# Kernel optimization log

Hardware: AMD Instinct MI355X
Metric: run time of the kernel (lower is better)

Reference implementation:

```python
import jax, jax.numpy as jnp
import numpy as np

N0, N1, N2 = 200000, 50000, 12500
E0, E1, E2 = 3200000, 800000, 200000
CIN, C, COUT = 4, 128, 1


def gcn(x, W, b, src, dst, n):
    # GCN conv with added self-loops and symmetric degree normalization
    h = x @ W
    loops = jnp.arange(n)
    s = jnp.concatenate([src, loops])
    d = jnp.concatenate([dst, loops])
    deg = jax.ops.segment_sum(jnp.ones(s.shape[0], h.dtype), d, num_segments=n)
    inv = jax.lax.rsqrt(jnp.maximum(deg, 1.0))
    msg = h[s] * (inv[s] * inv[d])[:, None]
    return jax.ops.segment_sum(msg, d, num_segments=n) + b


def pool_max(x, clusters, n_clusters):
    # cluster-based max pooling; empty clusters -> 0
    p = jax.ops.segment_max(x, clusters, num_segments=n_clusters)
    return jnp.where(jnp.isneginf(p), jnp.zeros_like(p), p)


def setup_inputs() -> dict:
    ks = jax.random.split(jax.random.key(0), 40)

    def w(k, i, o):
        return jax.random.normal(k, (i, o), jnp.float32) / np.float32(np.sqrt(i))

    inp = {
        'x': jax.random.normal(ks[0], (N0, CIN), jnp.float32),
        'edge_index0': jax.random.randint(ks[1], (2, E0), 0, N0),
        'edge_index1': jax.random.randint(ks[2], (2, E1), 0, N1),
        'edge_index2': jax.random.randint(ks[3], (2, E2), 0, N2),
        'clusters0': jax.random.randint(ks[4], (N0,), 0, N1),
        'clusters1': jax.random.randint(ks[5], (N1,), 0, N2),
        # encoder level 0
        'w_e0a': w(ks[6], CIN, C), 'b_e0a': jnp.zeros((C,), jnp.float32),
        'w_e0b': w(ks[7], C, C),   'b_e0b': jnp.zeros((C,), jnp.float32),
        # encoder level 1
        'w_e1a': w(ks[8], C, C),   'b_e1a': jnp.zeros((C,), jnp.float32),
        'w_e1b': w(ks[9], C, C),   'b_e1b': jnp.zeros((C,), jnp.float32),
        # bottom level 2
        'w_ba': w(ks[10], C, C),   'b_ba': jnp.zeros((C,), jnp.float32),
        'w_bb': w(ks[11], C, C),   'b_bb': jnp.zeros((C,), jnp.float32),
        # decoder level 1 (concat skip -> 2C in)
        'w_d1a': w(ks[12], 2 * C, C), 'b_d1a': jnp.zeros((C,), jnp.float32),
        'w_d1b': w(ks[13], C, C),     'b_d1b': jnp.zeros((C,), jnp.float32),
        # decoder level 0
        'w_d0a': w(ks[14], 2 * C, C), 'b_d0a': jnp.zeros((C,), jnp.float32),
        'w_d0b': w(ks[15], C, C),     'b_d0b': jnp.zeros((C,), jnp.float32),
        # output projection
        'w_out': w(ks[16], C, COUT), 'b_out': jnp.zeros((COUT,), jnp.float32),
    }
    return inp


def reference(x, edge_index0, edge_index1, edge_index2, clusters0, clusters1,
              w_e0a, b_e0a, w_e0b, b_e0b, w_e1a, b_e1a, w_e1b, b_e1b,
              w_ba, b_ba, w_bb, b_bb, w_d1a, b_d1a, w_d1b, b_d1b,
              w_d0a, b_d0a, w_d0b, b_d0b, w_out, b_out):
    n0 = x.shape[0]
    n1 = clusters1.shape[0]
    n2 = N2
    relu = jax.nn.relu
    s0, d0 = edge_index0[0], edge_index0[1]
    s1, d1 = edge_index1[0], edge_index1[1]
    s2, d2 = edge_index2[0], edge_index2[1]

    # encoder level 0
    e0 = relu(gcn(x, w_e0a, b_e0a, s0, d0, n0))
    e0 = relu(gcn(e0, w_e0b, b_e0b, s0, d0, n0))
    # pool -> level 1
    x1 = pool_max(e0, clusters0, n1)
    e1 = relu(gcn(x1, w_e1a, b_e1a, s1, d1, n1))
    e1 = relu(gcn(e1, w_e1b, b_e1b, s1, d1, n1))
    # pool -> level 2 (bottom)
    x2 = pool_max(e1, clusters1, n2)
    bt = relu(gcn(x2, w_ba, b_ba, s2, d2, n2))
    bt = relu(gcn(bt, w_bb, b_bb, s2, d2, n2))
    # unpool -> level 1, concat skip
    u1 = jnp.concatenate([bt[clusters1], e1], axis=1)
    dl1 = relu(gcn(u1, w_d1a, b_d1a, s1, d1, n1))
    dl1 = relu(gcn(dl1, w_d1b, b_d1b, s1, d1, n1))
    # unpool -> level 0, concat skip
    u0 = jnp.concatenate([dl1[clusters0], e0], axis=1)
    dl0 = relu(gcn(u0, w_d0a, b_d0a, s0, d0, n0))
    dl0 = relu(gcn(dl0, w_d0b, b_d0b, s0, d0, n0))
    # per-node output head
    return dl0 @ w_out + b_out
```

## Files before the change

### kernel.cpp

```cpp
#include <hip/hip_runtime.h>
#include <hip/hip_fp16.h>
#include <cstdint>
#include <cstddef>

#define PN0 200000
#define PN1 50000
#define PN2 12500
#define PE0 3200000
#define PE1 800000
#define PE2 200000

#define GCAP 64
#define CCAP 32

static inline int cdiv_i(int a, int b) { return (a + b - 1) / b; }

union H4 { uint4 q; uint2 u; __half2 h[2]; };

typedef _Float16 f16x8 __attribute__((ext_vector_type(8)));
typedef float f32x4 __attribute__((ext_vector_type(4)));
union F8 { uint4 q; f16x8 f; };

__device__ inline float2 load2f(const float* p) { return *(const float2*)p; }
__device__ inline float2 load2f(const __half* p) { return __half22float2(*(const __half2*)p); }


struct SegInfo {
    const int* idx[5];
    const int* src[3];
    int item_off[5];
    int cnt_off[5];
    int col_base[5];
    int cap[5];
    int total;
};

__global__ __launch_bounds__(256) void build_all_k(SegInfo s, int* __restrict__ cnt,
                                                   int* __restrict__ col) {
    int i = blockIdx.x * 256 + threadIdx.x;
    if (i >= s.total) return;
    int seg = 0;
#pragma unroll
    for (int t = 1; t < 5; ++t) if (i >= s.item_off[t]) seg = t;
    int il = i - s.item_off[seg];
    int d = s.idx[seg][il];
    int slot = atomicAdd(&cnt[s.cnt_off[seg] + d], 1);
    int cap = s.cap[seg];
    if (slot < cap) {
        int val = (seg < 3) ? s.src[seg][il] : il;
        col[s.col_base[seg] + d * cap + slot] = val;
    }
}

__global__ __launch_bounds__(256) void inv_all_k(const int* __restrict__ cnt, float* __restrict__ inv,
                                                 int c0, int c1, int c2) {
    int i = blockIdx.x * 256 + threadIdx.x;
    int total = PN0 + PN1 + PN2;
    if (i >= total) return;
    int coff, il;
    if (i < PN0) { coff = c0; il = i; }
    else if (i < PN0 + PN1) { coff = c1; il = i - PN0; }
    else { coff = c2; il = i - PN0 - PN1; }
    inv[i] = rsqrtf((float)(cnt[coff + il] + 1));
}

struct PrepW { const float* src[11]; __half* dst[11]; };
__global__ __launch_bounds__(256) void prep_w_k(PrepW p) {
    const float* w = p.src[blockIdx.x];
    __half* o = p.dst[blockIdx.x];
    for (int i = threadIdx.x; i < 16384; i += 256) {
        int k = i >> 7, n = i & 127;
        o[n * 128 + k] = __float2half(w[i]);
    }
}


__global__ __launch_bounds__(256) void agg4_k(const float* __restrict__ X, float* __restrict__ O,
                                              const int* __restrict__ deg, const int* __restrict__ col,
                                              const float* __restrict__ inv, int N) {
    int v = blockIdx.x * 256 + threadIdx.x;
    if (v >= N) return;
    float iv = inv[v];
    float4 xv = *(const float4*)(X + (size_t)v * 4);
    float ax = xv.x * iv, ay = xv.y * iv, az = xv.z * iv, aw = xv.w * iv;
    int b0 = v * GCAP, b1 = b0 + deg[v];
    for (int j = b0; j < b1; ++j) {
        int u = col[j];
        float iu = inv[u];
        float4 xu = *(const float4*)(X + (size_t)u * 4);
        ax += xu.x * iu; ay += xu.y * iu; az += xu.z * iu; aw += xu.w * iu;
    }
    float4 o; o.x = ax * iv; o.y = ay * iv; o.z = az * iv; o.w = aw * iv;
    *(float4*)(O + (size_t)v * 4) = o;
}

__global__ __launch_bounds__(256) void gemm4_k(const float* __restrict__ XA, const float* __restrict__ W,
                                               const float* __restrict__ bias, __half* __restrict__ O, int N) {
    int wid = (blockIdx.x * 256 + threadIdx.x) >> 6;
    int lane = threadIdx.x & 63;
    if (wid >= N) return;
    float4 x = *(const float4*)(XA + (size_t)wid * 4);
    int c = lane * 2;
    float2 w0 = *(const float2*)(W + c);
    float2 w1 = *(const float2*)(W + 128 + c);
    float2 w2 = *(const float2*)(W + 256 + c);
    float2 w3 = *(const float2*)(W + 384 + c);
    float2 b = *(const float2*)(bias + c);
    float ox = b.x + x.x * w0.x + x.y * w1.x + x.z * w2.x + x.w * w3.x;
    float oy = b.y + x.x * w0.y + x.y * w1.y + x.z * w2.y + x.w * w3.y;
    ox = fmaxf(ox, 0.f); oy = fmaxf(oy, 0.f);
    *(__half2*)(O + (size_t)wid * 128 + c) = __floats2half2_rn(ox, oy);
}

__global__ __launch_bounds__(256) void agg_k(const __half* __restrict__ H, __half* __restrict__ O,
                                             const int* __restrict__ deg, const int* __restrict__ col,
                                             const float* __restrict__ inv, const float* __restrict__ bias,
                                             int N) {
    int wpair = (blockIdx.x * 256 + threadIdx.x) >> 6;
    int lane = threadIdx.x & 63;
    int v = wpair * 2 + (lane >> 5);
    int l32 = lane & 31;
    if (v >= N) return;
    float iv = inv[v];
    int c4 = l32 * 4;
    float4 a0 = {0,0,0,0}, a1 = {0,0,0,0}, a2 = {0,0,0,0}, a3 = {0,0,0,0};
    int b0 = v * GCAP, b1 = b0 + deg[v];
    int j = b0;
    for (; j + 8 <= b1; j += 8) {
        int u0 = col[j],     u1 = col[j + 1], u2 = col[j + 2], u3 = col[j + 3];
        int u4 = col[j + 4], u5 = col[j + 5], u6 = col[j + 6], u7 = col[j + 7];
        H4 t0, t1, t2, t3, t4, t5, t6, t7;
        t0.u = *(const uint2*)(H + (size_t)u0 * 128 + c4);
        t1.u = *(const uint2*)(H + (size_t)u1 * 128 + c4);
        t2.u = *(const uint2*)(H + (size_t)u2 * 128 + c4);
        t3.u = *(const uint2*)(H + (size_t)u3 * 128 + c4);
        t4.u = *(const uint2*)(H + (size_t)u4 * 128 + c4);
        t5.u = *(const uint2*)(H + (size_t)u5 * 128 + c4);
        t6.u = *(const uint2*)(H + (size_t)u6 * 128 + c4);
        t7.u = *(const uint2*)(H + (size_t)u7 * 128 + c4);
        float2 p, q;
        p = __half22float2(t0.h[0]); q = __half22float2(t0.h[1]);
        a0.x += p.x; a0.y += p.y; a0.z += q.x; a0.w += q.y;
        p = __half22float2(t1.h[0]); q = __half22float2(t1.h[1]);
        a1.x += p.x; a1.y += p.y; a1.z += q.x; a1.w += q.y;
        p = __half22float2(t2.h[0]); q = __half22float2(t2.h[1]);
        a2.x += p.x; a2.y += p.y; a2.z += q.x; a2.w += q.y;
        p = __half22float2(t3.h[0]); q = __half22float2(t3.h[1]);
        a3.x += p.x; a3.y += p.y; a3.z += q.x; a3.w += q.y;
        p = __half22float2(t4.h[0]); q = __half22float2(t4.h[1]);
        a0.x += p.x; a0.y += p.y; a0.z += q.x; a0.w += q.y;
        p = __half22float2(t5.h[0]); q = __half22float2(t5.h[1]);
        a1.x += p.x; a1.y += p.y; a1.z += q.x; a1.w += q.y;
        p = __half22float2(t6.h[0]); q = __half22float2(t6.h[1]);
        a2.x += p.x; a2.y += p.y; a2.z += q.x; a2.w += q.y;
        p = __half22float2(t7.h[0]); q = __half22float2(t7.h[1]);
        a3.x += p.x; a3.y += p.y; a3.z += q.x; a3.w += q.y;
    }
    for (; j + 4 <= b1; j += 4) {
        int u0 = col[j], u1 = col[j + 1], u2 = col[j + 2], u3 = col[j + 3];
        H4 t0, t1, t2, t3;
        t0.u = *(const uint2*)(H + (size_t)u0 * 128 + c4);
        t1.u = *(const uint2*)(H + (size_t)u1 * 128 + c4);
        t2.u = *(const uint2*)(H + (size_t)u2 * 128 + c4);
        t3.u = *(const uint2*)(H + (size_t)u3 * 128 + c4);
        float2 p, q;
        p = __half22float2(t0.h[0]); q = __half22float2(t0.h[1]);
        a0.x += p.x; a0.y += p.y; a0.z += q.x; a0.w += q.y;
        p = __half22float2(t1.h[0]); q = __half22float2(t1.h[1]);
        a1.x += p.x; a1.y += p.y; a1.z += q.x; a1.w += q.y;
        p = __half22float2(t2.h[0]); q = __half22float2(t2.h[1]);
        a2.x += p.x; a2.y += p.y; a2.z += q.x; a2.w += q.y;
        p = __half22float2(t3.h[0]); q = __half22float2(t3.h[1]);
        a3.x += p.x; a3.y += p.y; a3.z += q.x; a3.w += q.y;
    }
    for (; j < b1; ++j) {
        H4 t; t.u = *(const uint2*)(H + (size_t)col[j] * 128 + c4);
        float2 p = __half22float2(t.h[0]), q = __half22float2(t.h[1]);
        a0.x += p.x; a0.y += p.y; a0.z += q.x; a0.w += q.y;
    }
    {
        H4 t; t.u = *(const uint2*)(H + (size_t)v * 128 + c4);
        float2 p = __half22float2(t.h[0]), q = __half22float2(t.h[1]);
        a1.x += p.x; a1.y += p.y; a1.z += q.x; a1.w += q.y;
    }
    float4 s;
    s.x = (a0.x + a1.x) + (a2.x + a3.x);
    s.y = (a0.y + a1.y) + (a2.y + a3.y);
    s.z = (a0.z + a1.z) + (a2.z + a3.z);
    s.w = (a0.w + a1.w) + (a2.w + a3.w);
    float4 b = *(const float4*)(bias + c4);
    H4 t;
    t.h[0] = __floats2half2_rn(fmaxf(s.x * iv + b.x, 0.f), fmaxf(s.y * iv + b.y, 0.f));
    t.h[1] = __floats2half2_rn(fmaxf(s.z * iv + b.z, 0.f), fmaxf(s.w * iv + b.w, 0.f));
    *(uint2*)(O + (size_t)v * 128 + c4) = t.u;
}

__global__ __launch_bounds__(256) void agg_head_k(const __half* __restrict__ H,
                                                  const int* __restrict__ deg, const int* __restrict__ col,
                                                  const float* __restrict__ inv, const float* __restrict__ bias,
                                                  const float* __restrict__ wout, const float* __restrict__ bout,
                                                  float* __restrict__ out, int N) {
    int wpair = (blockIdx.x * 256 + threadIdx.x) >> 6;
    int lane = threadIdx.x & 63;
    int v = wpair * 2 + (lane >> 5);
    int l32 = lane & 31;
    if (v >= N) return;
    float iv = inv[v];
    int c4 = l32 * 4;
    float4 a0 = {0,0,0,0}, a1 = {0,0,0,0}, a2 = {0,0,0,0}, a3 = {0,0,0,0};
    int b0 = v * GCAP, b1 = b0 + deg[v];
    int j = b0;
    for (; j + 8 <= b1; j += 8) {
        int u0 = col[j],     u1 = col[j + 1], u2 = col[j + 2], u3 = col[j + 3];
        int u4 = col[j + 4], u5 = col[j + 5], u6 = col[j + 6], u7 = col[j + 7];
        H4 t0, t1, t2, t3, t4, t5, t6, t7;
        t0.u = *(const uint2*)(H + (size_t)u0 * 128 + c4);
        t1.u = *(const uint2*)(H + (size_t)u1 * 128 + c4);
        t2.u = *(const uint2*)(H + (size_t)u2 * 128 + c4);
        t3.u = *(const uint2*)(H + (size_t)u3 * 128 + c4);
        t4.u = *(const uint2*)(H + (size_t)u4 * 128 + c4);
        t5.u = *(const uint2*)(H + (size_t)u5 * 128 + c4);
        t6.u = *(const uint2*)(H + (size_t)u6 * 128 + c4);
        t7.u = *(const uint2*)(H + (size_t)u7 * 128 + c4);
        float2 p, q;
        p = __half22float2(t0.h[0]); q = __half22float2(t0.h[1]);
        a0.x += p.x; a0.y += p.y; a0.z += q.x; a0.w += q.y;
        p = __half22float2(t1.h[0]); q = __half22float2(t1.h[1]);
        a1.x += p.x; a1.y += p.y; a1.z += q.x; a1.w += q.y;
        p = __half22float2(t2.h[0]); q = __half22float2(t2.h[1]);
        a2.x += p.x; a2.y += p.y; a2.z += q.x; a2.w += q.y;
        p = __half22float2(t3.h[0]); q = __half22float2(t3.h[1]);
        a3.x += p.x; a3.y += p.y; a3.z += q.x; a3.w += q.y;
        p = __half22float2(t4.h[0]); q = __half22float2(t4.h[1]);
        a0.x += p.x; a0.y += p.y; a0.z += q.x; a0.w += q.y;
        p = __half22float2(t5.h[0]); q = __half22float2(t5.h[1]);
        a1.x += p.x; a1.y += p.y; a1.z += q.x; a1.w += q.y;
        p = __half22float2(t6.h[0]); q = __half22float2(t6.h[1]);
        a2.x += p.x; a2.y += p.y; a2.z += q.x; a2.w += q.y;
        p = __half22float2(t7.h[0]); q = __half22float2(t7.h[1]);
        a3.x += p.x; a3.y += p.y; a3.z += q.x; a3.w += q.y;
    }
    for (; j + 4 <= b1; j += 4) {
        int u0 = col[j], u1 = col[j + 1], u2 = col[j + 2], u3 = col[j + 3];
        H4 t0, t1, t2, t3;
        t0.u = *(const uint2*)(H + (size_t)u0 * 128 + c4);
        t1.u = *(const uint2*)(H + (size_t)u1 * 128 + c4);
        t2.u = *(const uint2*)(H + (size_t)u2 * 128 + c4);
        t3.u = *(const uint2*)(H + (size_t)u3 * 128 + c4);
        float2 p, q;
        p = __half22float2(t0.h[0]); q = __half22float2(t0.h[1]);
        a0.x += p.x; a0.y += p.y; a0.z += q.x; a0.w += q.y;
        p = __half22float2(t1.h[0]); q = __half22float2(t1.h[1]);
        a1.x += p.x; a1.y += p.y; a1.z += q.x; a1.w += q.y;
        p = __half22float2(t2.h[0]); q = __half22float2(t2.h[1]);
        a2.x += p.x; a2.y += p.y; a2.z += q.x; a2.w += q.y;
        p = __half22float2(t3.h[0]); q = __half22float2(t3.h[1]);
        a3.x += p.x; a3.y += p.y; a3.z += q.x; a3.w += q.y;
    }
    for (; j < b1; ++j) {
        H4 t; t.u = *(const uint2*)(H + (size_t)col[j] * 128 + c4);
        float2 p = __half22float2(t.h[0]), q = __half22float2(t.h[1]);
        a0.x += p.x; a0.y += p.y; a0.z += q.x; a0.w += q.y;
    }
    {
        H4 t; t.u = *(const uint2*)(H + (size_t)v * 128 + c4);
        float2 p = __half22float2(t.h[0]), q = __half22float2(t.h[1]);
        a1.x += p.x; a1.y += p.y; a1.z += q.x; a1.w += q.y;
    }
    float4 sm;
    sm.x = (a0.x + a1.x) + (a2.x + a3.x);
    sm.y = (a0.y + a1.y) + (a2.y + a3.y);
    sm.z = (a0.z + a1.z) + (a2.z + a3.z);
    sm.w = (a0.w + a1.w) + (a2.w + a3.w);
    float4 b = *(const float4*)(bias + c4);
    float4 w = *(const float4*)(wout + c4);
    float s = fmaxf(sm.x * iv + b.x, 0.f) * w.x
            + fmaxf(sm.y * iv + b.y, 0.f) * w.y
            + fmaxf(sm.z * iv + b.z, 0.f) * w.z
            + fmaxf(sm.w * iv + b.w, 0.f) * w.w;
    for (int off = 16; off >= 1; off >>= 1) s += __shfl_down(s, off, 32);
    if (l32 == 0) out[v] = s + bout[0];
}

__global__ __launch_bounds__(256) void pool_k(const __half* __restrict__ X, __half* __restrict__ O,
                                              const int* __restrict__ cdeg, const int* __restrict__ col,
                                              int Nc) {
    int wid = (blockIdx.x * 256 + threadIdx.x) >> 6;
    int lane = threadIdx.x & 63;
    if (wid >= Nc) return;
    int c = lane * 2;
    float mx = 0.f, my = 0.f;
    int b0 = wid * CCAP, b1 = b0 + cdeg[wid];
    for (int j = b0; j < b1; ++j) {
        int u = col[j];
        float2 t = load2f(X + (size_t)u * 128 + c);
        mx = fmaxf(mx, t.x); my = fmaxf(my, t.y);
    }
    *(__half2*)(O + (size_t)wid * 128 + c) = __floats2half2_rn(mx, my);
}

__global__ __launch_bounds__(256) void gemm_mfma_k(const __half* __restrict__ X, const __half* __restrict__ Wt,
                                                   __half* __restrict__ O, int N,
                                                   const int* __restrict__ cl, const __half* __restrict__ T,
                                                   const float* __restrict__ rowscale) {
    __shared__ __half Ws[128 * 136];
    int tid = threadIdx.x;
    for (int i = tid; i < 2048; i += 256) {
        int n = i >> 4, k = (i & 15) * 8;
        *(uint4*)(&Ws[n * 136 + k]) = *(const uint4*)(Wt + n * 128 + k);
    }
    __syncthreads();

    int wave = tid >> 6, lane = tid & 63;
    int quad = lane >> 4, m = lane & 15;
    int rowBase = blockIdx.x * 64 + wave * 16;
    int arow = rowBase + m;
    bool aok = arow < N;

    f16x8 afr[4];
    const __half* xrow = X + (size_t)arow * 128;
#pragma unroll
    for (int kc = 0; kc < 4; ++kc) {
        F8 t;
        if (aok) t.q = *(const uint4*)(xrow + kc * 32 + quad * 8);
        else { t.q.x = 0; t.q.y = 0; t.q.z = 0; t.q.w = 0; }
        afr[kc] = t.f;
    }

    f32x4 acc[8];
#pragma unroll
    for (int t = 0; t < 8; ++t) acc[t] = (f32x4){0.f, 0.f, 0.f, 0.f};

#pragma unroll
    for (int kc = 0; kc < 4; ++kc) {
#pragma unroll
        for (int t = 0; t < 8; ++t) {
            F8 b;
            b.q = *(const uint4*)(&Ws[(t * 16 + m) * 136 + kc * 32 + quad * 8]);
            acc[t] = __builtin_amdgcn_mfma_f32_16x16x32_f16(afr[kc], b.f, acc[t], 0, 0, 0);
        }
    }

    int baseRow = rowBase + quad * 4;
#pragma unroll
    for (int r = 0; r < 4; ++r) {
        int orow = baseRow + r;
        if (orow >= N) continue;
        float rs = rowscale ? rowscale[orow] : 1.0f;
        const __half* Trow = cl ? (T + (size_t)cl[orow] * 128) : nullptr;
#pragma unroll
        for (int t = 0; t < 8; ++t) {
            float v = acc[t][r];
            if (Trow) v += __half2float(Trow[t * 16 + m]);
            O[(size_t)orow * 128 + t * 16 + m] = __float2half(v * rs);
        }
    }
}


extern "C" void kernel_launch(void* const* d_in, const int* in_sizes, int n_in,
                              void* d_out, int out_size, void* d_ws, size_t ws_size,
                              hipStream_t stream) {
    const float* x        = (const float*)d_in[0];
    const int*   ei0      = (const int*)d_in[1];
    const int*   ei1      = (const int*)d_in[2];
    const int*   ei2      = (const int*)d_in[3];
    const int*   cl0      = (const int*)d_in[4];
    const int*   cl1      = (const int*)d_in[5];
    const float* w_e0a = (const float*)d_in[6];  const float* b_e0a = (const float*)d_in[7];
    const float* w_e0b = (const float*)d_in[8];  const float* b_e0b = (const float*)d_in[9];
    const float* w_e1a = (const float*)d_in[10]; const float* b_e1a = (const float*)d_in[11];
    const float* w_e1b = (const float*)d_in[12]; const float* b_e1b = (const float*)d_in[13];
    const float* w_ba  = (const float*)d_in[14]; const float* b_ba  = (const float*)d_in[15];
    const float* w_bb  = (const float*)d_in[16]; const float* b_bb  = (const float*)d_in[17];
    const float* w_d1a = (const float*)d_in[18]; const float* b_d1a = (const float*)d_in[19];
    const float* w_d1b = (const float*)d_in[20]; const float* b_d1b = (const float*)d_in[21];
    const float* w_d0a = (const float*)d_in[22]; const float* b_d0a = (const float*)d_in[23];
    const float* w_d0b = (const float*)d_in[24]; const float* b_d0b = (const float*)d_in[25];
    const float* w_out = (const float*)d_in[26]; const float* b_out = (const float*)d_in[27];
    float* out = (float*)d_out;

    const int N0 = PN0, N1 = PN1, N2 = PN2;
    const int E0 = PE0, E1 = PE1, E2 = PE2;

    char* base = (char*)d_ws;
    size_t off = 0;
    auto alloc = [&](size_t bytes) -> char* {
        char* p = base + off;
        off += (bytes + 255) & ~(size_t)255;
        return p;
    };
    __half* bufA  = (__half*)alloc((size_t)N0 * 128 * 2);
    __half* h0    = (__half*)alloc((size_t)N0 * 128 * 2);
    __half* h16   = (__half*)alloc((size_t)N1 * 128 * 2);
    __half* e1buf = (__half*)alloc((size_t)N1 * 128 * 2);
    __half* x1buf = (__half*)alloc((size_t)N1 * 128 * 2);
    __half* x2buf = (__half*)alloc((size_t)N2 * 128 * 2);
    __half* btbuf = (__half*)alloc((size_t)N2 * 128 * 2);
    __half* t2    = (__half*)alloc((size_t)N2 * 128 * 2);
    __half* t3    = (__half*)alloc((size_t)N1 * 128 * 2);
    float*  xa4   = (float*)alloc((size_t)N0 * 4 * 4);
    float*  INV   = (float*)alloc((size_t)(N0 + N1 + N2) * 4);
    const int c0 = 0, c1g = N0, c2g = c1g + N1, c3g = c2g + N2, c4g = c3g + N1;
    const int cntLen = c4g + N2;
    int* CNT = (int*)alloc((size_t)cntLen * 4);
    const int o0 = 0, o1 = N0 * GCAP, o2 = o1 + N1 * GCAP, o3 = o2 + N2 * GCAP, o4 = o3 + N1 * CCAP;
    const int colLen = o4 + N2 * CCAP;
    int* COL = (int*)alloc((size_t)colLen * 4);
    __half* WT = (__half*)alloc((size_t)11 * 128 * 128 * 2);
    if (off > ws_size) return;

    float* inv0 = INV;
    float* inv1 = INV + N0;
    float* inv2 = INV + N0 + N1;
    int* deg0 = CNT + c0;  int* col0 = COL + o0;
    int* deg1 = CNT + c1g; int* col1 = COL + o1;
    int* deg2 = CNT + c2g; int* col2 = COL + o2;
    int* cdeg0 = CNT + c3g; int* ccol0 = COL + o3;
    int* cdeg1 = CNT + c4g; int* ccol1 = COL + o4;

    (void)n_in; (void)in_sizes; (void)out_size;

    hipMemsetAsync(CNT, 0, (size_t)cntLen * 4, stream);
    const int totalItems = E0 + E1 + E2 + N0 + N1;
    SegInfo si;
    si.idx[0] = ei0 + E0; si.idx[1] = ei1 + E1; si.idx[2] = ei2 + E2;
    si.idx[3] = cl0;      si.idx[4] = cl1;
    si.src[0] = ei0; si.src[1] = ei1; si.src[2] = ei2;
    si.item_off[0] = 0;       si.item_off[1] = E0;          si.item_off[2] = E0 + E1;
    si.item_off[3] = E0 + E1 + E2; si.item_off[4] = E0 + E1 + E2 + N0;
    si.cnt_off[0] = c0;  si.cnt_off[1] = c1g; si.cnt_off[2] = c2g;
    si.cnt_off[3] = c3g; si.cnt_off[4] = c4g;
    si.col_base[0] = o0; si.col_base[1] = o1; si.col_base[2] = o2;
    si.col_base[3] = o3; si.col_base[4] = o4;
    si.cap[0] = GCAP; si.cap[1] = GCAP; si.cap[2] = GCAP; si.cap[3] = CCAP; si.cap[4] = CCAP;
    si.total = totalItems;
    build_all_k<<<cdiv_i(totalItems, 256), 256, 0, stream>>>(si, CNT, COL);
    inv_all_k<<<cdiv_i(N0 + N1 + N2, 256), 256, 0, stream>>>(CNT, INV, c0, c1g, c2g);

    __half* wt_e0b = WT;                __half* wt_e1a = WT + 16384;
    __half* wt_e1b = WT + 2 * 16384;    __half* wt_ba  = WT + 3 * 16384;
    __half* wt_bb  = WT + 4 * 16384;    __half* wt_d1aT = WT + 5 * 16384;
    __half* wt_d1aB = WT + 6 * 16384;   __half* wt_d1b = WT + 7 * 16384;
    __half* wt_d0aT = WT + 8 * 16384;   __half* wt_d0aB = WT + 9 * 16384;
    __half* wt_d0b = WT + 10 * 16384;
    PrepW pw;
    pw.src[0] = w_e0b;  pw.dst[0] = wt_e0b;
    pw.src[1] = w_e1a;  pw.dst[1] = wt_e1a;
    pw.src[2] = w_e1b;  pw.dst[2] = wt_e1b;
    pw.src[3] = w_ba;   pw.dst[3] = wt_ba;
    pw.src[4] = w_bb;   pw.dst[4] = wt_bb;
    pw.src[5] = w_d1a;            pw.dst[5] = wt_d1aT;
    pw.src[6] = w_d1a + 16384;    pw.dst[6] = wt_d1aB;
    pw.src[7] = w_d1b;  pw.dst[7] = wt_d1b;
    pw.src[8] = w_d0a;            pw.dst[8] = wt_d0aT;
    pw.src[9] = w_d0a + 16384;    pw.dst[9] = wt_d0aB;
    pw.src[10] = w_d0b; pw.dst[10] = wt_d0b;
    prep_w_k<<<11, 256, 0, stream>>>(pw);

    auto mfma = [&](const __half* X, const __half* Wt, __half* O, int N,
                    const int* cl, const __half* T, const float* rs) {
        gemm_mfma_k<<<cdiv_i(N, 64), 256, 0, stream>>>(X, Wt, O, N, cl, T, rs);
    };
    auto agg = [&](const __half* H, __half* O, const int* deg, const int* col, const float* inv,
                   const float* bias, int N) {
        agg_k<<<cdiv_i(N, 8), 256, 0, stream>>>(H, O, deg, col, inv, bias, N);
    };

    agg4_k<<<cdiv_i(N0, 256), 256, 0, stream>>>(x, xa4, deg0, col0, inv0, N0);
    gemm4_k<<<cdiv_i(N0, 4), 256, 0, stream>>>(xa4, w_e0a, b_e0a, bufA, N0);
    mfma(bufA, wt_e0b, h0, N0, nullptr, nullptr, inv0);
    agg(h0, bufA, deg0, col0, inv0, b_e0b, N0);
    pool_k<<<cdiv_i(N1, 4), 256, 0, stream>>>(bufA, x1buf, cdeg0, ccol0, N1);
    mfma(x1buf, wt_e1a, h16, N1, nullptr, nullptr, inv1);
    agg(h16, e1buf, deg1, col1, inv1, b_e1a, N1);
    mfma(e1buf, wt_e1b, h16, N1, nullptr, nullptr, inv1);
    agg(h16, e1buf, deg1, col1, inv1, b_e1b, N1);
    pool_k<<<cdiv_i(N2, 4), 256, 0, stream>>>(e1buf, x2buf, cdeg1, ccol1, N2);
    mfma(x2buf, wt_ba, h16, N2, nullptr, nullptr, inv2);
    agg(h16, btbuf, deg2, col2, inv2, b_ba, N2);
    mfma(btbuf, wt_bb, h16, N2, nullptr, nullptr, inv2);
    agg(h16, btbuf, deg2, col2, inv2, b_bb, N2);
    mfma(btbuf, wt_d1aT, t2, N2, nullptr, nullptr, nullptr);
    mfma(e1buf, wt_d1aB, h16, N1, cl1, t2, inv1);
    agg(h16, x1buf, deg1, col1, inv1, b_d1a, N1);
    mfma(x1buf, wt_d1b, h16, N1, nullptr, nullptr, inv1);
    agg(h16, x1buf, deg1, col1, inv1, b_d1b, N1);
    mfma(x1buf, wt_d0aT, t3, N1, nullptr, nullptr, nullptr);
    mfma(bufA, wt_d0aB, h0, N0, cl0, t3, inv0);
    agg(h0, bufA, deg0, col0, inv0, b_d0a, N0);
    mfma(bufA, wt_d0b, h0, N0, nullptr, nullptr, inv0);
    agg_head_k<<<cdiv_i(N0, 8), 256, 0, stream>>>(h0, deg0, col0, inv0, b_d0b,
                                                  w_out, b_out, out, N0);
}
```

Before: 1.262 ms.

## Build adjacency via bucketed counting sort instead of global atomics

```diff
diff --git a/kernel.cpp b/kernel.cpp
--- a/kernel.cpp
+++ b/kernel.cpp
@@ -13,6 +13,17 @@
 #define GCAP 64
 #define CCAP 32
 
+#define P0 0
+#define P1 200192
+#define P2 250368
+#define P3 263168
+#define P4 313344
+#define CNT_END 326144
+#define NBUCKETS 637
+#define NITEMS 4450000
+#define IPB 8192
+#define NBLK 544
+
 static inline int cdiv_i(int a, int b) { return (a + b - 1) / b; }
 
 union H4 { uint4 q; uint2 u; __half2 h[2]; };
@@ -25,43 +36,149 @@
 __device__ inline float2 load2f(const __half* p) { return __half22float2(*(const __half2*)p); }
 
 
-struct SegInfo {
+struct BSeg {
     const int* idx[5];
     const int* src[3];
     int item_off[5];
-    int cnt_off[5];
-    int col_base[5];
+    int P[5];
+    int colb[5];
     int cap[5];
-    int total;
+    int nN[5];
+    int ioff[3];
 };
 
-__global__ __launch_bounds__(256) void build_all_k(SegInfo s, int* __restrict__ cnt,
-                                                   int* __restrict__ col) {
-    int i = blockIdx.x * 256 + threadIdx.x;
-    if (i >= s.total) return;
+__device__ inline int seg_of_item(const BSeg& s, int i) {
     int seg = 0;
 #pragma unroll
     for (int t = 1; t < 5; ++t) if (i >= s.item_off[t]) seg = t;
-    int il = i - s.item_off[seg];
-    int d = s.idx[seg][il];
-    int slot = atomicAdd(&cnt[s.cnt_off[seg] + d], 1);
-    int cap = s.cap[seg];
-    if (slot < cap) {
-        int val = (seg < 3) ? s.src[seg][il] : il;
-        col[s.col_base[seg] + d * cap + slot] = val;
-    }
-}
-
-__global__ __launch_bounds__(256) void inv_all_k(const int* __restrict__ cnt, float* __restrict__ inv,
-                                                 int c0, int c1, int c2) {
-    int i = blockIdx.x * 256 + threadIdx.x;
-    int total = PN0 + PN1 + PN2;
-    if (i >= total) return;
-    int coff, il;
-    if (i < PN0) { coff = c0; il = i; }
-    else if (i < PN0 + PN1) { coff = c1; il = i - PN0; }
-    else { coff = c2; il = i - PN0 - PN1; }
-    inv[i] = rsqrtf((float)(cnt[coff + il] + 1));
+    return seg;
+}
+__device__ inline int seg_of_g(const BSeg& s, int g) {
+    int seg = 0;
+#pragma unroll
+    for (int t = 1; t < 5; ++t) if (g >= s.P[t]) seg = t;
+    return seg;
+}
+
+__global__ __launch_bounds__(256) void hist_k(BSeg s, int* __restrict__ BH) {
+    __shared__ int lh[640];
+    int tid = threadIdx.x;
+    for (int k = tid; k < 640; k += 256) lh[k] = 0;
+    __syncthreads();
+    int base = blockIdx.x * IPB;
+#pragma unroll 4
+    for (int it = 0; it < 32; ++it) {
+        int i = base + it * 256 + tid;
+        if (i < NITEMS) {
+            int seg = seg_of_item(s, i);
+            int il = i - s.item_off[seg];
+            int g = s.P[seg] + s.idx[seg][il];
+            atomicAdd(&lh[g >> 9], 1);
+        }
+    }
+    __syncthreads();
+    for (int k = tid; k < 640; k += 256) BH[blockIdx.x * 640 + k] = lh[k];
+}
+
+__global__ __launch_bounds__(256) void scan_bh_k(int* __restrict__ BH, int* __restrict__ BT) {
+    int b = blockIdx.x;
+    int tid = threadIdx.x;
+    __shared__ int tsum[256];
+    int v[3];
+    int base = tid * 3;
+    int sum = 0;
+#pragma unroll
+    for (int k = 0; k < 3; ++k) {
+        int idx = base + k;
+        v[k] = (idx < NBLK) ? BH[idx * 640 + b] : 0;
+        sum += v[k];
+    }
+    tsum[tid] = sum;
+    __syncthreads();
+    for (int off = 1; off < 256; off <<= 1) {
+        int t = (tid >= off) ? tsum[tid - off] : 0;
+        __syncthreads();
+        tsum[tid] += t;
+        __syncthreads();
+    }
+    int excl = tsum[tid] - sum;
+#pragma unroll
+    for (int k = 0; k < 3; ++k) {
+        int idx = base + k;
+        if (idx < NBLK) { BH[idx * 640 + b] = excl; excl += v[k]; }
+    }
+    if (tid == 255) BT[b] = tsum[255];
+}
+
+__global__ __launch_bounds__(1024) void bb_scan_k(const int* __restrict__ BT, int* __restrict__ BB) {
+    __shared__ int sm[1024];
+    int tid = threadIdx.x;
+    int v = (tid < NBUCKETS) ? BT[tid] : 0;
+    sm[tid] = v;
+    __syncthreads();
+    for (int off = 1; off < 1024; off <<= 1) {
+        int t = (tid >= off) ? sm[tid - off] : 0;
+        __syncthreads();
+        sm[tid] += t;
+        __syncthreads();
+    }
+    if (tid < NBUCKETS) BB[tid] = sm[tid] - v;
+}
+
+__global__ __launch_bounds__(256) void scatter_k(BSeg s, const int* __restrict__ BH,
+                                                 const int* __restrict__ BB, int2* __restrict__ sorted) {
+    __shared__ int lr[640];
+    int tid = threadIdx.x;
+    for (int k = tid; k < 640; k += 256) lr[k] = 0;
+    __syncthreads();
+    int base = blockIdx.x * IPB;
+#pragma unroll 4
+    for (int it = 0; it < 32; ++it) {
+        int i = base + it * 256 + tid;
+        if (i < NITEMS) {
+            int seg = seg_of_item(s, i);
+            int il = i - s.item_off[seg];
+            int g = s.P[seg] + s.idx[seg][il];
+            int val = (seg < 3) ? s.src[seg][il] : il;
+            int b = g >> 9;
+            int r = atomicAdd(&lr[b], 1);
+            int pos = BB[b] + BH[blockIdx.x * 640 + b] + r;
+            sorted[pos] = make_int2(g, val);
+        }
+    }
+}
+
+__global__ __launch_bounds__(256) void buildc_k(BSeg s, const int2* __restrict__ sorted,
+                                                const int* __restrict__ BB, const int* __restrict__ BT,
+                                                int* __restrict__ col, int* __restrict__ cnt,
+                                                float* __restrict__ inv) {
+    int b = blockIdx.x;
+    int tid = threadIdx.x;
+    __shared__ int lc[512];
+    for (int k = tid; k < 512; k += 256) lc[k] = 0;
+    __syncthreads();
+    int start = BB[b], end = start + BT[b];
+    for (int i = start + tid; i < end; i += 256) {
+        int2 p = sorted[i];
+        int g = p.x;
+        int local = g & 511;
+        int slot = atomicAdd(&lc[local], 1);
+        int seg = seg_of_g(s, g);
+        int d = g - s.P[seg];
+        int cap = s.cap[seg];
+        if (slot < cap) col[s.colb[seg] + d * cap + slot] = p.y;
+    }
+    __syncthreads();
+    for (int local = tid; local < 512; local += 256) {
+        int g = (b << 9) + local;
+        int seg = seg_of_g(s, g);
+        int d = g - s.P[seg];
+        if (d < s.nN[seg]) {
+            int c = lc[local];
+            cnt[g] = c;
+            if (seg < 3) inv[s.ioff[seg] + d] = rsqrtf((float)(c + 1));
+        }
+    }
 }
 
 struct PrepW { const float* src[11]; __half* dst[11]; };
@@ -401,42 +518,46 @@
     __half* t3    = (__half*)alloc((size_t)N1 * 128 * 2);
     float*  xa4   = (float*)alloc((size_t)N0 * 4 * 4);
     float*  INV   = (float*)alloc((size_t)(N0 + N1 + N2) * 4);
-    const int c0 = 0, c1g = N0, c2g = c1g + N1, c3g = c2g + N2, c4g = c3g + N1;
-    const int cntLen = c4g + N2;
-    int* CNT = (int*)alloc((size_t)cntLen * 4);
+    int* CNT = (int*)alloc((size_t)CNT_END * 4);
     const int o0 = 0, o1 = N0 * GCAP, o2 = o1 + N1 * GCAP, o3 = o2 + N2 * GCAP, o4 = o3 + N1 * CCAP;
     const int colLen = o4 + N2 * CCAP;
     int* COL = (int*)alloc((size_t)colLen * 4);
     __half* WT = (__half*)alloc((size_t)11 * 128 * 128 * 2);
+    int* BT = (int*)alloc(640 * 4);
+    int* BB = (int*)alloc(640 * 4);
     if (off > ws_size) return;
+
+    int2* sorted = (int2*)h0;
+    int*  BH     = (int*)h16;
 
     float* inv0 = INV;
     float* inv1 = INV + N0;
     float* inv2 = INV + N0 + N1;
-    int* deg0 = CNT + c0;  int* col0 = COL + o0;
-    int* deg1 = CNT + c1g; int* col1 = COL + o1;
-    int* deg2 = CNT + c2g; int* col2 = COL + o2;
-    int* cdeg0 = CNT + c3g; int* ccol0 = COL + o3;
-    int* cdeg1 = CNT + c4g; int* ccol1 = COL + o4;
+    int* deg0 = CNT + P0;  int* col0 = COL + o0;
+    int* deg1 = CNT + P1;  int* col1 = COL + o1;
+    int* deg2 = CNT + P2;  int* col2 = COL + o2;
+    int* cdeg0 = CNT + P3; int* ccol0 = COL + o3;
+    int* cdeg1 = CNT + P4; int* ccol1 = COL + o4;
 
     (void)n_in; (void)in_sizes; (void)out_size;
 
-    hipMemsetAsync(CNT, 0, (size_t)cntLen * 4, stream);
-    const int totalItems = E0 + E1 + E2 + N0 + N1;
-    SegInfo si;
-    si.idx[0] = ei0 + E0; si.idx[1] = ei1 + E1; si.idx[2] = ei2 + E2;
-    si.idx[3] = cl0;      si.idx[4] = cl1;
-    si.src[0] = ei0; si.src[1] = ei1; si.src[2] = ei2;
-    si.item_off[0] = 0;       si.item_off[1] = E0;          si.item_off[2] = E0 + E1;
-    si.item_off[3] = E0 + E1 + E2; si.item_off[4] = E0 + E1 + E2 + N0;
-    si.cnt_off[0] = c0;  si.cnt_off[1] = c1g; si.cnt_off[2] = c2g;
-    si.cnt_off[3] = c3g; si.cnt_off[4] = c4g;
-    si.col_base[0] = o0; si.col_base[1] = o1; si.col_base[2] = o2;
-    si.col_base[3] = o3; si.col_base[4] = o4;
-    si.cap[0] = GCAP; si.cap[1] = GCAP; si.cap[2] = GCAP; si.cap[3] = CCAP; si.cap[4] = CCAP;
-    si.total = totalItems;
-    build_all_k<<<cdiv_i(totalItems, 256), 256, 0, stream>>>(si, CNT, COL);
-    inv_all_k<<<cdiv_i(N0 + N1 + N2, 256), 256, 0, stream>>>(CNT, INV, c0, c1g, c2g);
+    BSeg bs;
+    bs.idx[0] = ei0 + E0; bs.idx[1] = ei1 + E1; bs.idx[2] = ei2 + E2;
+    bs.idx[3] = cl0;      bs.idx[4] = cl1;
+    bs.src[0] = ei0; bs.src[1] = ei1; bs.src[2] = ei2;
+    bs.item_off[0] = 0;            bs.item_off[1] = E0;                bs.item_off[2] = E0 + E1;
+    bs.item_off[3] = E0 + E1 + E2; bs.item_off[4] = E0 + E1 + E2 + N0;
+    bs.P[0] = P0; bs.P[1] = P1; bs.P[2] = P2; bs.P[3] = P3; bs.P[4] = P4;
+    bs.colb[0] = o0; bs.colb[1] = o1; bs.colb[2] = o2; bs.colb[3] = o3; bs.colb[4] = o4;
+    bs.cap[0] = GCAP; bs.cap[1] = GCAP; bs.cap[2] = GCAP; bs.cap[3] = CCAP; bs.cap[4] = CCAP;
+    bs.nN[0] = N0; bs.nN[1] = N1; bs.nN[2] = N2; bs.nN[3] = N1; bs.nN[4] = N2;
+    bs.ioff[0] = 0; bs.ioff[1] = N0; bs.ioff[2] = N0 + N1;
+
+    hist_k<<<NBLK, 256, 0, stream>>>(bs, BH);
+    scan_bh_k<<<NBUCKETS, 256, 0, stream>>>(BH, BT);
+    bb_scan_k<<<1, 1024, 0, stream>>>(BT, BB);
+    scatter_k<<<NBLK, 256, 0, stream>>>(bs, BH, BB, sorted);
+    buildc_k<<<NBUCKETS, 256, 0, stream>>>(bs, sorted, BB, BT, COL, CNT, INV);
 
     __half* wt_e0b = WT;                __half* wt_e1a = WT + 16384;
     __half* wt_e1b = WT + 2 * 16384;    __half* wt_ba  = WT + 3 * 16384;
```

New measurement: 1.190 ms (median of 2 runs). 5.7% less time.
